# Kernel tuning notes

Measured on AMD Instinct MI355X. Metric: run time of the kernel, lower is better.

## Reference

```python
import jax, jax.numpy as jnp
import numpy as np

B, S, D = 2, 2048, 1024
E, K, F = 8, 2, 4 * D


def setup_inputs() -> dict:
    key = jax.random.key(0)
    ks = jax.random.split(key, 5)
    sd = 1.0 / np.sqrt(D)
    sf = 1.0 / np.sqrt(F)
    x = jax.random.normal(ks[0], (B, S, D), dtype=jnp.float32)
    Wg = jax.random.uniform(ks[1], (D, E), dtype=jnp.float32, minval=-sd, maxval=sd)
    W1 = jax.random.uniform(ks[2], (E, D, F), dtype=jnp.float32, minval=-sd, maxval=sd)
    W3 = jax.random.uniform(ks[3], (D, E * F), dtype=jnp.float32, minval=-sd, maxval=sd).reshape(D, E, F).transpose(1, 0, 2)
    W2 = jax.random.uniform(ks[4], (E, F, D), dtype=jnp.float32, minval=-sf, maxval=sf)
    return {"x": x, "Wg": Wg, "W1": W1, "W2": W2, "W3": W3}


def reference(x, Wg, W1, W2, W3):
    Bx, Sx, Dx = x.shape
    xf = x.reshape(-1, Dx)  # [T, D]
    T = xf.shape[0]
    gate_logits = xf @ Wg  # [T, E]
    probs = jax.nn.softmax(gate_logits, axis=-1)
    weights, sel = jax.lax.top_k(probs, K)  # [T, K]
    weights = weights / jnp.sum(weights, axis=-1, keepdims=True)
    # scatter top-k weights into a dense [T, E] combine matrix (top-k indices are distinct)
    coef = jnp.zeros((T, W1.shape[0]), dtype=xf.dtype)
    coef = coef.at[jnp.arange(T)[:, None], sel].add(weights)
    out = jnp.zeros_like(xf)
    for e in range(W1.shape[0]):  # small fixed expert count
        h = jax.nn.silu(xf @ W1[e]) * (xf @ W3[e])  # [T, F]
        out = out + coef[:, e:e + 1] * (h @ W2[e])
    aux_loss = jnp.mean(jnp.var(gate_logits, axis=-1, ddof=1))  # torch .var() is unbiased
    return out.reshape(Bx, Sx, Dx), aux_loss
```

## Files before the change

kernel.cpp:

```cpp
#include <hip/hip_runtime.h>

typedef __bf16 bf16x8 __attribute__((ext_vector_type(8)));
typedef float  f32x4  __attribute__((ext_vector_type(4)));

#define TOKS 4096
#define DIM  1024
#define NEXP 8
#define NF   4096
#define CAP  4096
#define BM 128
#define BN 128
#define BK 64

__device__ __forceinline__ unsigned short f2bf(float f) {
  unsigned int u = __float_as_uint(f);
  u += 0x7FFFu + ((u >> 16) & 1u);
  return (unsigned short)(u >> 16);
}
__device__ __forceinline__ int swzo(int major) {
  return ((major & 7) ^ ((major >> 3) & 7)) << 3;
}
__device__ __forceinline__ int swz8(int row, int chunk) {
  return (chunk ^ (row & 7)) << 3;
}

__global__ void moe_route(const float* __restrict__ x, const float* __restrict__ Wg,
                          int* __restrict__ pairCnt, int* __restrict__ pairIdx,
                          float* __restrict__ pairWgt, float* __restrict__ auxSum)
{
  int lane = threadIdx.x & 63;
  int tok  = blockIdx.x * 4 + (threadIdx.x >> 6);
  const float* xr = x + (size_t)tok * DIM;
  float acc[8];
  #pragma unroll
  for (int e = 0; e < 8; ++e) acc[e] = 0.f;
  #pragma unroll
  for (int i = 0; i < 16; ++i) {
    int d = i * 64 + lane;
    float xv = xr[d];
    const float4* wr = (const float4*)(Wg + d * 8);
    float4 wa = wr[0], wb = wr[1];
    acc[0] += xv * wa.x; acc[1] += xv * wa.y; acc[2] += xv * wa.z; acc[3] += xv * wa.w;
    acc[4] += xv * wb.x; acc[5] += xv * wb.y; acc[6] += xv * wb.z; acc[7] += xv * wb.w;
  }
  #pragma unroll
  for (int e = 0; e < 8; ++e) {
    float v = acc[e];
    #pragma unroll
    for (int off = 32; off; off >>= 1) v += __shfl_xor(v, off);
    acc[e] = v;
  }
  if (lane == 0) {
    int e1 = 0; float l1 = acc[0];
    #pragma unroll
    for (int e = 1; e < 8; ++e) if (acc[e] > l1) { l1 = acc[e]; e1 = e; }
    int e2 = -1; float l2 = -3.4e38f;
    #pragma unroll
    for (int e = 0; e < 8; ++e) if (e != e1 && acc[e] > l2) { l2 = acc[e]; e2 = e; }
    float r  = expf(l2 - l1);
    float w1 = 1.f / (1.f + r);
    float w2 = r / (1.f + r);
    int s1 = atomicAdd(&pairCnt[e1], 1);
    pairIdx[e1 * CAP + s1] = tok * 2;     pairWgt[e1 * CAP + s1] = w1;
    int s2 = atomicAdd(&pairCnt[e2], 1);
    pairIdx[e2 * CAP + s2] = tok * 2 + 1; pairWgt[e2 * CAP + s2] = w2;
    float m = 0.f;
    #pragma unroll
    for (int e = 0; e < 8; ++e) m += acc[e];
    m *= 0.125f;
    float v = 0.f;
    #pragma unroll
    for (int e = 0; e < 8; ++e) { float dd = acc[e] - m; v += dd * dd; }
    atomicAdd(auxSum, v * (1.f / 7.f));
  }
}

__global__ void moe_aux_final(const float* __restrict__ auxSum, float* __restrict__ outScalar) {
  *outScalar = auxSum[0] * (1.f / (float)TOKS);
}

__global__ __launch_bounds__(256) void cvt_transpose(
    const float* __restrict__ in, unsigned short* __restrict__ outp, int R, int C)
{
  __shared__ unsigned short tile[64 * 72];
  int e  = blockIdx.z;
  int r0 = blockIdx.x * 64, c0 = blockIdx.y * 64;
  const float*    ine  = in   + (size_t)e * R * C;
  unsigned short* oute = outp + (size_t)e * R * C;
  int t = threadIdx.x;
  int r = t >> 2, cs = (t & 3) * 16;
  const float4* src = (const float4*)(ine + (size_t)(r0 + r) * C + c0 + cs);
  #pragma unroll
  for (int j = 0; j < 4; ++j) {
    float4 v = src[j];
    tile[(cs + j * 4 + 0) * 72 + r] = f2bf(v.x);
    tile[(cs + j * 4 + 1) * 72 + r] = f2bf(v.y);
    tile[(cs + j * 4 + 2) * 72 + r] = f2bf(v.z);
    tile[(cs + j * 4 + 3) * 72 + r] = f2bf(v.w);
  }
  __syncthreads();
  int c = t >> 2, rs = (t & 3) * 16;
  uint4 o0 = *(const uint4*)&tile[c * 72 + rs];
  uint4 o1 = *(const uint4*)&tile[c * 72 + rs + 8];
  unsigned short* dst = oute + (size_t)(c0 + c) * R + r0 + rs;
  *(uint4*)dst       = o0;
  *(uint4*)(dst + 8) = o1;
}

__global__ __launch_bounds__(512) void moe_ffn1_f(
    const float* __restrict__ x, const unsigned short* __restrict__ W1T,
    const unsigned short* __restrict__ W3T,
    const int* __restrict__ pairCnt, const int* __restrict__ pairIdx,
    unsigned short* __restrict__ hbuf)
{
  int bid = blockIdx.x;
  int m_t = (bid >> 3) & 31;
  int n_t = (bid & 7) | (((bid >> 8) & 3) << 3);
  int e   = bid >> 10;
  int cnt = pairCnt[e];
  int m0  = m_t * BM;
  if (m0 >= cnt) return;
  int n0  = n_t * BN;
  __shared__ __attribute__((aligned(16))) unsigned short As[BM * BK];
  __shared__ __attribute__((aligned(16))) unsigned short B1s[BN * BK];
  __shared__ __attribute__((aligned(16))) unsigned short B3s[BN * BK];
  __shared__ int rowPid[BM];
  int tid = threadIdx.x;
  if (tid < BM) {
    int gi = m0 + tid;
    rowPid[tid] = (gi < cnt) ? pairIdx[e * CAP + gi] : -1;
  }
  const unsigned short* W1e = W1T + (size_t)e * NF * DIM + (size_t)n0 * DIM;
  const unsigned short* W3e = W3T + (size_t)e * NF * DIM + (size_t)n0 * DIM;
  f32x4 zero = {0.f, 0.f, 0.f, 0.f};
  f32x4 acc1[2][4], acc2[2][4];
  #pragma unroll
  for (int mi = 0; mi < 2; ++mi)
    #pragma unroll
    for (int ni = 0; ni < 4; ++ni) { acc1[mi][ni] = zero; acc2[mi][ni] = zero; }
  int lane = tid & 63, wid = tid >> 6;
  int wm = (wid >> 1) * 32, wn = (wid & 1) * 64;

  int sr = tid >> 2;
  int sc = (tid & 3) * 16;
  int co = sc >> 3;
  __syncthreads();
  int pidA = rowPid[sr];
  const float* xrow = x + (size_t)((pidA >= 0) ? (pidA >> 1) : 0) * DIM + sc;
  const unsigned short* b1row = W1e + (size_t)sr * DIM + sc;
  const unsigned short* b3row = W3e + (size_t)sr * DIM + sc;

  for (int kt = 0; kt < DIM; kt += BK) {
    {
      const float4* xs = (const float4*)(xrow + kt);
      float4 v0 = xs[0], v1 = xs[1], v2 = xs[2], v3 = xs[3];
      union { unsigned short u[8]; uint4 q; } p0, p1;
      p0.u[0]=f2bf(v0.x); p0.u[1]=f2bf(v0.y); p0.u[2]=f2bf(v0.z); p0.u[3]=f2bf(v0.w);
      p0.u[4]=f2bf(v1.x); p0.u[5]=f2bf(v1.y); p0.u[6]=f2bf(v1.z); p0.u[7]=f2bf(v1.w);
      p1.u[0]=f2bf(v2.x); p1.u[1]=f2bf(v2.y); p1.u[2]=f2bf(v2.z); p1.u[3]=f2bf(v2.w);
      p1.u[4]=f2bf(v3.x); p1.u[5]=f2bf(v3.y); p1.u[6]=f2bf(v3.z); p1.u[7]=f2bf(v3.w);
      *(uint4*)&As[sr * BK + swz8(sr, co)]     = p0.q;
      *(uint4*)&As[sr * BK + swz8(sr, co + 1)] = p1.q;
    }
    {
      uint4 q0 = *(const uint4*)(b1row + kt);
      uint4 q1 = *(const uint4*)(b1row + kt + 8);
      uint4 r0 = *(const uint4*)(b3row + kt);
      uint4 r1 = *(const uint4*)(b3row + kt + 8);
      *(uint4*)&B1s[sr * BK + swz8(sr, co)]     = q0;
      *(uint4*)&B1s[sr * BK + swz8(sr, co + 1)] = q1;
      *(uint4*)&B3s[sr * BK + swz8(sr, co)]     = r0;
      *(uint4*)&B3s[sr * BK + swz8(sr, co + 1)] = r1;
    }
    __syncthreads();
    #pragma unroll
    for (int ks = 0; ks < 2; ++ks) {
      int kc = ks * 4 + (lane >> 4);
      bf16x8 af[2];
      #pragma unroll
      for (int mi = 0; mi < 2; ++mi) {
        int row = wm + mi * 16 + (lane & 15);
        af[mi] = *(const bf16x8*)(&As[row * BK + swz8(row, kc)]);
      }
      #pragma unroll
      for (int ni = 0; ni < 4; ++ni) {
        int f = wn + ni * 16 + (lane & 15);
        bf16x8 b1 = *(const bf16x8*)(&B1s[f * BK + swz8(f, kc)]);
        bf16x8 b3 = *(const bf16x8*)(&B3s[f * BK + swz8(f, kc)]);
        #pragma unroll
        for (int mi = 0; mi < 2; ++mi) {
          acc1[mi][ni] = __builtin_amdgcn_mfma_f32_16x16x32_bf16(af[mi], b1, acc1[mi][ni], 0, 0, 0);
          acc2[mi][ni] = __builtin_amdgcn_mfma_f32_16x16x32_bf16(af[mi], b3, acc2[mi][ni], 0, 0, 0);
        }
      }
    }
    __syncthreads();
  }
  #pragma unroll
  for (int mi = 0; mi < 2; ++mi) {
    #pragma unroll
    for (int r = 0; r < 4; ++r) {
      int row = wm + mi * 16 + ((lane >> 4) << 2) + r;
      int pid = rowPid[row];
      if (pid < 0) continue;
      size_t hb = (size_t)pid * NF + n0 + wn + (lane & 15);
      #pragma unroll
      for (int ni = 0; ni < 4; ++ni) {
        float a = acc1[mi][ni][r];
        float g = acc2[mi][ni][r];
        float s = 1.f / (1.f + __expf(-a));
        hbuf[hb + ni * 16] = f2bf(a * s * g);
      }
    }
  }
}

__global__ __launch_bounds__(512) void moe_ffn2_f(
    const unsigned short* __restrict__ hbuf, const unsigned short* __restrict__ W2T,
    const int* __restrict__ pairCnt, const int* __restrict__ pairIdx,
    const float* __restrict__ pairWgt, float* __restrict__ out)
{
  int bid = blockIdx.x;
  int n_t = bid & 7;
  int m_t = (bid >> 3) & 31;
  int e   = bid >> 8;
  int cnt = pairCnt[e];
  int m0  = m_t * BM;
  if (m0 >= cnt) return;
  int n0  = n_t * BN;
  __shared__ __attribute__((aligned(16))) unsigned short As[BM * BK];
  __shared__ __attribute__((aligned(16))) unsigned short Bs[BN * BK];
  __shared__ int   rowPid[BM];
  __shared__ float rowW[BM];
  int tid = threadIdx.x;
  if (tid < BM) {
    int gi = m0 + tid;
    if (gi < cnt) { rowPid[tid] = pairIdx[e * CAP + gi]; rowW[tid] = pairWgt[e * CAP + gi]; }
    else          { rowPid[tid] = -1;                    rowW[tid] = 0.f; }
  }
  const unsigned short* W2e = W2T + (size_t)e * DIM * NF + (size_t)n0 * NF;
  f32x4 zero = {0.f, 0.f, 0.f, 0.f};
  f32x4 acc[2][4];
  #pragma unroll
  for (int mi = 0; mi < 2; ++mi)
    #pragma unroll
    for (int ni = 0; ni < 4; ++ni) acc[mi][ni] = zero;
  int lane = tid & 63, wid = tid >> 6;
  int wm = (wid >> 1) * 32, wn = (wid & 1) * 64;

  int sr = tid >> 2;
  int sc = (tid & 3) * 16;
  int co = sc >> 3;
  __syncthreads();
  int pidA = rowPid[sr];
  const unsigned short* hrow = hbuf + (size_t)((pidA >= 0) ? pidA : 0) * NF + sc;
  const unsigned short* brow = W2e + (size_t)sr * NF + sc;

  for (int kt = 0; kt < NF; kt += BK) {
    {
      uint4 a0 = *(const uint4*)(hrow + kt);
      uint4 a1 = *(const uint4*)(hrow + kt + 8);
      uint4 q0 = *(const uint4*)(brow + kt);
      uint4 q1 = *(const uint4*)(brow + kt + 8);
      *(uint4*)&As[sr * BK + swz8(sr, co)]     = a0;
      *(uint4*)&As[sr * BK + swz8(sr, co + 1)] = a1;
      *(uint4*)&Bs[sr * BK + swz8(sr, co)]     = q0;
      *(uint4*)&Bs[sr * BK + swz8(sr, co + 1)] = q1;
    }
    __syncthreads();
    #pragma unroll
    for (int ks = 0; ks < 2; ++ks) {
      int kc = ks * 4 + (lane >> 4);
      bf16x8 af[2];
      #pragma unroll
      for (int mi = 0; mi < 2; ++mi) {
        int row = wm + mi * 16 + (lane & 15);
        af[mi] = *(const bf16x8*)(&As[row * BK + swz8(row, kc)]);
      }
      #pragma unroll
      for (int ni = 0; ni < 4; ++ni) {
        int dc = wn + ni * 16 + (lane & 15);
        bf16x8 b = *(const bf16x8*)(&Bs[dc * BK + swz8(dc, kc)]);
        #pragma unroll
        for (int mi = 0; mi < 2; ++mi)
          acc[mi][ni] = __builtin_amdgcn_mfma_f32_16x16x32_bf16(af[mi], b, acc[mi][ni], 0, 0, 0);
      }
    }
    __syncthreads();
  }
  #pragma unroll
  for (int mi = 0; mi < 2; ++mi) {
    #pragma unroll
    for (int r = 0; r < 4; ++r) {
      int row = wm + mi * 16 + ((lane >> 4) << 2) + r;
      int pid = rowPid[row];
      if (pid < 0) continue;
      float w = rowW[row];
      float* op = out + (size_t)(pid >> 1) * DIM + n0 + wn + (lane & 15);
      #pragma unroll
      for (int ni = 0; ni < 4; ++ni)
        atomicAdd(op + ni * 16, w * acc[mi][ni][r]);
    }
  }
}

__global__ __launch_bounds__(512) void moe_ffn1(
    const float* __restrict__ x, const float* __restrict__ W1, const float* __restrict__ W3,
    const int* __restrict__ pairCnt, const int* __restrict__ pairIdx,
    unsigned short* __restrict__ hbuf)
{
  int e   = blockIdx.z;
  int cnt = pairCnt[e];
  int m0  = blockIdx.x * BM;
  if (m0 >= cnt) return;
  int n0  = blockIdx.y * BN;
  __shared__ __attribute__((aligned(16))) unsigned short As[BM * BK];
  __shared__ __attribute__((aligned(16))) unsigned short B1s[BN * BK];
  __shared__ __attribute__((aligned(16))) unsigned short B3s[BN * BK];
  __shared__ int rowPid[BM];
  int tid = threadIdx.x;
  if (tid < BM) {
    int gi = m0 + tid;
    rowPid[tid] = (gi < cnt) ? pairIdx[e * CAP + gi] : -1;
  }
  const float* W1e = W1 + (size_t)e * DIM * NF;
  const float* W3e = W3 + (size_t)e * DIM * NF;
  f32x4 zero = {0.f, 0.f, 0.f, 0.f};
  f32x4 acc1[2][4], acc2[2][4];
  #pragma unroll
  for (int mi = 0; mi < 2; ++mi)
    #pragma unroll
    for (int ni = 0; ni < 4; ++ni) { acc1[mi][ni] = zero; acc2[mi][ni] = zero; }
  int lane = tid & 63, wid = tid >> 6;
  int wm = (wid >> 1) * 32, wn = (wid & 1) * 64;

  for (int kt = 0; kt < DIM; kt += BK) {
    __syncthreads();
    #pragma unroll
    for (int it = 0; it < 4; ++it) {
      int row = it * 32 + (tid >> 4);
      int dq  = tid & 15;
      int pid = rowPid[row];
      int tk  = (pid >= 0) ? (pid >> 1) : 0;
      float4 v = *(const float4*)(x + (size_t)tk * DIM + kt + dq * 4);
      ushort4 b; b.x = f2bf(v.x); b.y = f2bf(v.y); b.z = f2bf(v.z); b.w = f2bf(v.w);
      *(ushort4*)(&As[row * BK + ((dq * 4) ^ swzo(row))]) = b;
    }
    #pragma unroll
    for (int it = 0; it < 4; ++it) {
      int d  = it * 16 + (tid >> 5);
      int fq = tid & 31;
      size_t go = (size_t)(kt + d) * NF + n0 + fq * 4;
      float4 v1 = *(const float4*)(W1e + go);
      float4 v3 = *(const float4*)(W3e + go);
      const float* p1 = (const float*)&v1;
      const float* p3 = (const float*)&v3;
      #pragma unroll
      for (int i = 0; i < 4; ++i) {
        int f   = fq * 4 + i;
        int idx = f * BK + (d ^ swzo(f));
        B1s[idx] = f2bf(p1[i]);
        B3s[idx] = f2bf(p3[i]);
      }
    }
    __syncthreads();
    #pragma unroll
    for (int ks = 0; ks < 2; ++ks) {
      int kb = ks * 32 + ((lane >> 4) << 3);
      bf16x8 af[2];
      #pragma unroll
      for (int mi = 0; mi < 2; ++mi) {
        int row = wm + mi * 16 + (lane & 15);
        af[mi] = *(const bf16x8*)(&As[row * BK + (kb ^ swzo(row))]);
      }
      #pragma unroll
      for (int ni = 0; ni < 4; ++ni) {
        int f = wn + ni * 16 + (lane & 15);
        bf16x8 b1 = *(const bf16x8*)(&B1s[f * BK + (kb ^ swzo(f))]);
        bf16x8 b3 = *(const bf16x8*)(&B3s[f * BK + (kb ^ swzo(f))]);
        #pragma unroll
        for (int mi = 0; mi < 2; ++mi) {
          acc1[mi][ni] = __builtin_amdgcn_mfma_f32_16x16x32_bf16(af[mi], b1, acc1[mi][ni], 0, 0, 0);
          acc2[mi][ni] = __builtin_amdgcn_mfma_f32_16x16x32_bf16(af[mi], b3, acc2[mi][ni], 0, 0, 0);
        }
      }
    }
  }
  #pragma unroll
  for (int mi = 0; mi < 2; ++mi) {
    #pragma unroll
    for (int r = 0; r < 4; ++r) {
      int row = wm + mi * 16 + ((lane >> 4) << 2) + r;
      int pid = rowPid[row];
      if (pid < 0) continue;
      size_t hb = (size_t)pid * NF + n0 + wn + (lane & 15);
      #pragma unroll
      for (int ni = 0; ni < 4; ++ni) {
        float a = acc1[mi][ni][r];
        float g = acc2[mi][ni][r];
        float s = 1.f / (1.f + __expf(-a));
        hbuf[hb + ni * 16] = f2bf(a * s * g);
      }
    }
  }
}

__global__ __launch_bounds__(512) void moe_ffn2(
    const unsigned short* __restrict__ hbuf, const float* __restrict__ W2,
    const int* __restrict__ pairCnt, const int* __restrict__ pairIdx,
    const float* __restrict__ pairWgt, float* __restrict__ out)
{
  int e   = blockIdx.z;
  int cnt = pairCnt[e];
  int m0  = blockIdx.x * BM;
  if (m0 >= cnt) return;
  int n0  = blockIdx.y * BN;
  __shared__ __attribute__((aligned(16))) unsigned short As[BM * BK];
  __shared__ __attribute__((aligned(16))) unsigned short Bs[BN * BK];
  __shared__ int   rowPid[BM];
  __shared__ float rowW[BM];
  int tid = threadIdx.x;
  if (tid < BM) {
    int gi = m0 + tid;
    if (gi < cnt) { rowPid[tid] = pairIdx[e * CAP + gi]; rowW[tid] = pairWgt[e * CAP + gi]; }
    else          { rowPid[tid] = -1;                    rowW[tid] = 0.f; }
  }
  const float* W2e = W2 + (size_t)e * NF * DIM;
  f32x4 zero = {0.f, 0.f, 0.f, 0.f};
  f32x4 acc[2][4];
  #pragma unroll
  for (int mi = 0; mi < 2; ++mi)
    #pragma unroll
    for (int ni = 0; ni < 4; ++ni) acc[mi][ni] = zero;
  int lane = tid & 63, wid = tid >> 6;
  int wm = (wid >> 1) * 32, wn = (wid & 1) * 64;

  for (int kt = 0; kt < NF; kt += BK) {
    __syncthreads();
    #pragma unroll
    for (int it = 0; it < 2; ++it) {
      int row = it * 64 + (tid >> 3);
      int c8  = tid & 7;
      int pid = rowPid[row];
      int pr  = (pid >= 0) ? pid : 0;
      uint4 v = *(const uint4*)(hbuf + (size_t)pr * NF + kt + c8 * 8);
      *(uint4*)(&As[row * BK + ((c8 * 8) ^ swzo(row))]) = v;
    }
    #pragma unroll
    for (int it = 0; it < 4; ++it) {
      int fk = it * 16 + (tid >> 5);
      int dq = tid & 31;
      float4 v = *(const float4*)(W2e + (size_t)(kt + fk) * DIM + n0 + dq * 4);
      const float* p = (const float*)&v;
      #pragma unroll
      for (int i = 0; i < 4; ++i) {
        int dc = dq * 4 + i;
        Bs[dc * BK + (fk ^ swzo(dc))] = f2bf(p[i]);
      }
    }
    __syncthreads();
    #pragma unroll
    for (int ks = 0; ks < 2; ++ks) {
      int kb = ks * 32 + ((lane >> 4) << 3);
      bf16x8 af[2];
      #pragma unroll
      for (int mi = 0; mi < 2; ++mi) {
        int row = wm + mi * 16 + (lane & 15);
        af[mi] = *(const bf16x8*)(&As[row * BK + (kb ^ swzo(row))]);
      }
      #pragma unroll
      for (int ni = 0; ni < 4; ++ni) {
        int dc = wn + ni * 16 + (lane & 15);
        bf16x8 b = *(const bf16x8*)(&Bs[dc * BK + (kb ^ swzo(dc))]);
        #pragma unroll
        for (int mi = 0; mi < 2; ++mi)
          acc[mi][ni] = __builtin_amdgcn_mfma_f32_16x16x32_bf16(af[mi], b, acc[mi][ni], 0, 0, 0);
      }
    }
  }
  #pragma unroll
  for (int mi = 0; mi < 2; ++mi) {
    #pragma unroll
    for (int r = 0; r < 4; ++r) {
      int row = wm + mi * 16 + ((lane >> 4) << 2) + r;
      int pid = rowPid[row];
      if (pid < 0) continue;
      float w = rowW[row];
      float* op = out + (size_t)(pid >> 1) * DIM + n0 + wn + (lane & 15);
      #pragma unroll
      for (int ni = 0; ni < 4; ++ni)
        atomicAdd(op + ni * 16, w * acc[mi][ni][r]);
    }
  }
}

extern "C" void kernel_launch(void* const* d_in, const int* in_sizes, int n_in,
                              void* d_out, int out_size, void* d_ws, size_t ws_size,
                              hipStream_t stream)
{
  const float* x  = (const float*)d_in[0];
  const float* Wg = (const float*)d_in[1];
  const float* W1 = (const float*)d_in[2];
  const float* W2 = (const float*)d_in[3];
  const float* W3 = (const float*)d_in[4];
  float* out = (float*)d_out;
  char*  ws  = (char*)d_ws;
  int*   pairCnt = (int*)ws;
  float* auxSum  = (float*)(ws + 64);
  int*   pairIdx = (int*)(ws + 4096);
  float* pairWgt = (float*)(ws + 262144);
  unsigned short* hbuf = (unsigned short*)(ws + ((size_t)1 << 20));
  unsigned short* W1T  = (unsigned short*)(ws + ((size_t)68 << 20));
  unsigned short* W3T  = (unsigned short*)(ws + ((size_t)132 << 20));
  unsigned short* W2T  = (unsigned short*)(ws + ((size_t)196 << 20));
  const size_t WS_NEED = (size_t)260 << 20;

  hipMemsetAsync(ws, 0, 128, stream);
  hipMemsetAsync(d_out, 0, (size_t)out_size * sizeof(float), stream);
  moe_route<<<TOKS / 4, 256, 0, stream>>>(x, Wg, pairCnt, pairIdx, pairWgt, auxSum);
  moe_aux_final<<<1, 1, 0, stream>>>(auxSum, out + (out_size - 1));

  if (ws_size >= WS_NEED) {
    cvt_transpose<<<dim3(DIM / 64, NF / 64, NEXP), 256, 0, stream>>>(W1, W1T, DIM, NF);
    cvt_transpose<<<dim3(DIM / 64, NF / 64, NEXP), 256, 0, stream>>>(W3, W3T, DIM, NF);
    cvt_transpose<<<dim3(NF / 64, DIM / 64, NEXP), 256, 0, stream>>>(W2, W2T, NF, DIM);
    moe_ffn1_f<<<(TOKS / BM) * (NF / BN) * NEXP, 512, 0, stream>>>(x, W1T, W3T, pairCnt, pairIdx, hbuf);
    moe_ffn2_f<<<(TOKS / BM) * (DIM / BN) * NEXP, 512, 0, stream>>>(hbuf, W2T, pairCnt, pairIdx, pairWgt, out);
  } else {
    moe_ffn1<<<dim3(TOKS / BM, NF / BN, NEXP), 512, 0, stream>>>(x, W1, W3, pairCnt, pairIdx, hbuf);
    moe_ffn2<<<dim3(TOKS / BM, DIM / BN, NEXP), 512, 0, stream>>>(hbuf, W2, pairCnt, pairIdx, pairWgt, out);
  }
}
```

Measured before the change: 618.3 us.

## Pre-convert x to bf16 and stage GEMM tiles with direct global-to-LDS loads

```diff
diff --git a/kernel.cpp b/kernel.cpp
--- a/kernel.cpp
+++ b/kernel.cpp
@@ -11,6 +11,12 @@
 #define BM 128
 #define BN 128
 #define BK 64
+
+typedef __attribute__((address_space(3))) unsigned int as3_u32;
+typedef __attribute__((address_space(1))) unsigned int as1_u32;
+__device__ __forceinline__ void gl16(const unsigned short* g, unsigned short* l) {
+  __builtin_amdgcn_global_load_lds((as1_u32*)(unsigned long long)g, (as3_u32*)l, 16, 0, 0);
+}
 
 __device__ __forceinline__ unsigned short f2bf(float f) {
   unsigned int u = __float_as_uint(f);
@@ -79,6 +85,21 @@
   *outScalar = auxSum[0] * (1.f / (float)TOKS);
 }
 
+__global__ __launch_bounds__(256) void cvt_x(const float* __restrict__ in,
+                                             unsigned short* __restrict__ o)
+{
+  int i = (blockIdx.x * 256 + threadIdx.x) * 16;
+  const float4* s = (const float4*)(in + i);
+  float4 a = s[0], b = s[1], c = s[2], d = s[3];
+  union { unsigned short u[8]; uint4 q; } p0, p1;
+  p0.u[0]=f2bf(a.x); p0.u[1]=f2bf(a.y); p0.u[2]=f2bf(a.z); p0.u[3]=f2bf(a.w);
+  p0.u[4]=f2bf(b.x); p0.u[5]=f2bf(b.y); p0.u[6]=f2bf(b.z); p0.u[7]=f2bf(b.w);
+  p1.u[0]=f2bf(c.x); p1.u[1]=f2bf(c.y); p1.u[2]=f2bf(c.z); p1.u[3]=f2bf(c.w);
+  p1.u[4]=f2bf(d.x); p1.u[5]=f2bf(d.y); p1.u[6]=f2bf(d.z); p1.u[7]=f2bf(d.w);
+  *(uint4*)(o + i)     = p0.q;
+  *(uint4*)(o + i + 8) = p1.q;
+}
+
 __global__ __launch_bounds__(256) void cvt_transpose(
     const float* __restrict__ in, unsigned short* __restrict__ outp, int R, int C)
 {
@@ -107,8 +128,8 @@
   *(uint4*)(dst + 8) = o1;
 }
 
-__global__ __launch_bounds__(512) void moe_ffn1_f(
-    const float* __restrict__ x, const unsigned short* __restrict__ W1T,
+__global__ __launch_bounds__(512) void moe_ffn1_g(
+    const unsigned short* __restrict__ xbf, const unsigned short* __restrict__ W1T,
     const unsigned short* __restrict__ W3T,
     const int* __restrict__ pairCnt, const int* __restrict__ pairIdx,
     unsigned short* __restrict__ hbuf)
@@ -125,7 +146,7 @@
   __shared__ __attribute__((aligned(16))) unsigned short B1s[BN * BK];
   __shared__ __attribute__((aligned(16))) unsigned short B3s[BN * BK];
   __shared__ int rowPid[BM];
-  int tid = threadIdx.x;
+  int tid = threadIdx.x, lane = tid & 63, wid = tid >> 6;
   if (tid < BM) {
     int gi = m0 + tid;
     rowPid[tid] = (gi < cnt) ? pairIdx[e * CAP + gi] : -1;
@@ -138,40 +159,32 @@
   for (int mi = 0; mi < 2; ++mi)
     #pragma unroll
     for (int ni = 0; ni < 4; ++ni) { acc1[mi][ni] = zero; acc2[mi][ni] = zero; }
-  int lane = tid & 63, wid = tid >> 6;
   int wm = (wid >> 1) * 32, wn = (wid & 1) * 64;
-
-  int sr = tid >> 2;
-  int sc = (tid & 3) * 16;
-  int co = sc >> 3;
   __syncthreads();
-  int pidA = rowPid[sr];
-  const float* xrow = x + (size_t)((pidA >= 0) ? (pidA >> 1) : 0) * DIM + sc;
-  const unsigned short* b1row = W1e + (size_t)sr * DIM + sc;
-  const unsigned short* b3row = W3e + (size_t)sr * DIM + sc;
+
+  int r0a = wid * 16 + (lane >> 3), r1a = r0a + 8;
+  int p0 = rowPid[r0a], p1 = rowPid[r1a];
+  size_t tk0 = (size_t)((p0 >= 0) ? (p0 >> 1) : 0);
+  size_t tk1 = (size_t)((p1 >= 0) ? (p1 >> 1) : 0);
+  int ch0 = ((lane & 7) ^ (r0a & 7)) * 8;
+  int ch1 = ((lane & 7) ^ (r1a & 7)) * 8;
+  const unsigned short* gA0  = xbf + tk0 * DIM + ch0;
+  const unsigned short* gA1  = xbf + tk1 * DIM + ch1;
+  const unsigned short* gB10 = W1e + (size_t)r0a * DIM + ch0;
+  const unsigned short* gB11 = W1e + (size_t)r1a * DIM + ch1;
+  const unsigned short* gB30 = W3e + (size_t)r0a * DIM + ch0;
+  const unsigned short* gB31 = W3e + (size_t)r1a * DIM + ch1;
+  unsigned short* lA0  = &As [(wid * 16) * BK];
+  unsigned short* lA1  = &As [(wid * 16 + 8) * BK];
+  unsigned short* lB10 = &B1s[(wid * 16) * BK];
+  unsigned short* lB11 = &B1s[(wid * 16 + 8) * BK];
+  unsigned short* lB30 = &B3s[(wid * 16) * BK];
+  unsigned short* lB31 = &B3s[(wid * 16 + 8) * BK];
 
   for (int kt = 0; kt < DIM; kt += BK) {
-    {
-      const float4* xs = (const float4*)(xrow + kt);
-      float4 v0 = xs[0], v1 = xs[1], v2 = xs[2], v3 = xs[3];
-      union { unsigned short u[8]; uint4 q; } p0, p1;
-      p0.u[0]=f2bf(v0.x); p0.u[1]=f2bf(v0.y); p0.u[2]=f2bf(v0.z); p0.u[3]=f2bf(v0.w);
-      p0.u[4]=f2bf(v1.x); p0.u[5]=f2bf(v1.y); p0.u[6]=f2bf(v1.z); p0.u[7]=f2bf(v1.w);
-      p1.u[0]=f2bf(v2.x); p1.u[1]=f2bf(v2.y); p1.u[2]=f2bf(v2.z); p1.u[3]=f2bf(v2.w);
-      p1.u[4]=f2bf(v3.x); p1.u[5]=f2bf(v3.y); p1.u[6]=f2bf(v3.z); p1.u[7]=f2bf(v3.w);
-      *(uint4*)&As[sr * BK + swz8(sr, co)]     = p0.q;
-      *(uint4*)&As[sr * BK + swz8(sr, co + 1)] = p1.q;
-    }
-    {
-      uint4 q0 = *(const uint4*)(b1row + kt);
-      uint4 q1 = *(const uint4*)(b1row + kt + 8);
-      uint4 r0 = *(const uint4*)(b3row + kt);
-      uint4 r1 = *(const uint4*)(b3row + kt + 8);
-      *(uint4*)&B1s[sr * BK + swz8(sr, co)]     = q0;
-      *(uint4*)&B1s[sr * BK + swz8(sr, co + 1)] = q1;
-      *(uint4*)&B3s[sr * BK + swz8(sr, co)]     = r0;
-      *(uint4*)&B3s[sr * BK + swz8(sr, co + 1)] = r1;
-    }
+    gl16(gA0 + kt, lA0);  gl16(gA1 + kt, lA1);
+    gl16(gB10 + kt, lB10); gl16(gB11 + kt, lB11);
+    gl16(gB30 + kt, lB30); gl16(gB31 + kt, lB31);
     __syncthreads();
     #pragma unroll
     for (int ks = 0; ks < 2; ++ks) {
@@ -215,7 +228,7 @@
   }
 }
 
-__global__ __launch_bounds__(512) void moe_ffn2_f(
+__global__ __launch_bounds__(512) void moe_ffn2_g(
     const unsigned short* __restrict__ hbuf, const unsigned short* __restrict__ W2T,
     const int* __restrict__ pairCnt, const int* __restrict__ pairIdx,
     const float* __restrict__ pairWgt, float* __restrict__ out)
@@ -232,7 +245,7 @@
   __shared__ __attribute__((aligned(16))) unsigned short Bs[BN * BK];
   __shared__ int   rowPid[BM];
   __shared__ float rowW[BM];
-  int tid = threadIdx.x;
+  int tid = threadIdx.x, lane = tid & 63, wid = tid >> 6;
   if (tid < BM) {
     int gi = m0 + tid;
     if (gi < cnt) { rowPid[tid] = pairIdx[e * CAP + gi]; rowW[tid] = pairWgt[e * CAP + gi]; }
@@ -245,28 +258,27 @@
   for (int mi = 0; mi < 2; ++mi)
     #pragma unroll
     for (int ni = 0; ni < 4; ++ni) acc[mi][ni] = zero;
-  int lane = tid & 63, wid = tid >> 6;
   int wm = (wid >> 1) * 32, wn = (wid & 1) * 64;
-
-  int sr = tid >> 2;
-  int sc = (tid & 3) * 16;
-  int co = sc >> 3;
   __syncthreads();
-  int pidA = rowPid[sr];
-  const unsigned short* hrow = hbuf + (size_t)((pidA >= 0) ? pidA : 0) * NF + sc;
-  const unsigned short* brow = W2e + (size_t)sr * NF + sc;
+
+  int r0a = wid * 16 + (lane >> 3), r1a = r0a + 8;
+  int p0 = rowPid[r0a], p1 = rowPid[r1a];
+  size_t h0 = (size_t)((p0 >= 0) ? p0 : 0);
+  size_t h1 = (size_t)((p1 >= 0) ? p1 : 0);
+  int ch0 = ((lane & 7) ^ (r0a & 7)) * 8;
+  int ch1 = ((lane & 7) ^ (r1a & 7)) * 8;
+  const unsigned short* gA0 = hbuf + h0 * NF + ch0;
+  const unsigned short* gA1 = hbuf + h1 * NF + ch1;
+  const unsigned short* gB0 = W2e + (size_t)r0a * NF + ch0;
+  const unsigned short* gB1 = W2e + (size_t)r1a * NF + ch1;
+  unsigned short* lA0 = &As[(wid * 16) * BK];
+  unsigned short* lA1 = &As[(wid * 16 + 8) * BK];
+  unsigned short* lB0 = &Bs[(wid * 16) * BK];
+  unsigned short* lB1 = &Bs[(wid * 16 + 8) * BK];
 
   for (int kt = 0; kt < NF; kt += BK) {
-    {
-      uint4 a0 = *(const uint4*)(hrow + kt);
-      uint4 a1 = *(const uint4*)(hrow + kt + 8);
-      uint4 q0 = *(const uint4*)(brow + kt);
-      uint4 q1 = *(const uint4*)(brow + kt + 8);
-      *(uint4*)&As[sr * BK + swz8(sr, co)]     = a0;
-      *(uint4*)&As[sr * BK + swz8(sr, co + 1)] = a1;
-      *(uint4*)&Bs[sr * BK + swz8(sr, co)]     = q0;
-      *(uint4*)&Bs[sr * BK + swz8(sr, co + 1)] = q1;
-    }
+    gl16(gA0 + kt, lA0); gl16(gA1 + kt, lA1);
+    gl16(gB0 + kt, lB0); gl16(gB1 + kt, lB1);
     __syncthreads();
     #pragma unroll
     for (int ks = 0; ks < 2; ++ks) {
@@ -509,11 +521,12 @@
   float* auxSum  = (float*)(ws + 64);
   int*   pairIdx = (int*)(ws + 4096);
   float* pairWgt = (float*)(ws + 262144);
-  unsigned short* hbuf = (unsigned short*)(ws + ((size_t)1 << 20));
-  unsigned short* W1T  = (unsigned short*)(ws + ((size_t)68 << 20));
-  unsigned short* W3T  = (unsigned short*)(ws + ((size_t)132 << 20));
-  unsigned short* W2T  = (unsigned short*)(ws + ((size_t)196 << 20));
-  const size_t WS_NEED = (size_t)260 << 20;
+  unsigned short* xbf  = (unsigned short*)(ws + ((size_t)1 << 20));
+  unsigned short* hbuf = (unsigned short*)(ws + ((size_t)9 << 20));
+  unsigned short* W1T  = (unsigned short*)(ws + ((size_t)73 << 20));
+  unsigned short* W3T  = (unsigned short*)(ws + ((size_t)137 << 20));
+  unsigned short* W2T  = (unsigned short*)(ws + ((size_t)201 << 20));
+  const size_t WS_NEED = (size_t)265 << 20;
 
   hipMemsetAsync(ws, 0, 128, stream);
   hipMemsetAsync(d_out, 0, (size_t)out_size * sizeof(float), stream);
@@ -521,11 +534,12 @@
   moe_aux_final<<<1, 1, 0, stream>>>(auxSum, out + (out_size - 1));
 
   if (ws_size >= WS_NEED) {
+    cvt_x<<<TOKS * DIM / (256 * 16), 256, 0, stream>>>(x, xbf);
     cvt_transpose<<<dim3(DIM / 64, NF / 64, NEXP), 256, 0, stream>>>(W1, W1T, DIM, NF);
     cvt_transpose<<<dim3(DIM / 64, NF / 64, NEXP), 256, 0, stream>>>(W3, W3T, DIM, NF);
     cvt_transpose<<<dim3(NF / 64, DIM / 64, NEXP), 256, 0, stream>>>(W2, W2T, NF, DIM);
-    moe_ffn1_f<<<(TOKS / BM) * (NF / BN) * NEXP, 512, 0, stream>>>(x, W1T, W3T, pairCnt, pairIdx, hbuf);
-    moe_ffn2_f<<<(TOKS / BM) * (DIM / BN) * NEXP, 512, 0, stream>>>(hbuf, W2T, pairCnt, pairIdx, pairWgt, out);
+    moe_ffn1_g<<<(TOKS / BM) * (NF / BN) * NEXP, 512, 0, stream>>>(xbf, W1T, W3T, pairCnt, pairIdx, hbuf);
+    moe_ffn2_g<<<(TOKS / BM) * (DIM / BN) * NEXP, 512, 0, stream>>>(hbuf, W2T, pairCnt, pairIdx, pairWgt, out);
   } else {
     moe_ffn1<<<dim3(TOKS / BM, NF / BN, NEXP), 512, 0, stream>>>(x, W1, W3, pairCnt, pairIdx, hbuf);
     moe_ffn2<<<dim3(TOKS / BM, DIM / BN, NEXP), 512, 0, stream>>>(hbuf, W2, pairCnt, pairIdx, pairWgt, out);
```

New measurement: 545.1 us. 1.13x faster.
